# Performance work log

Measured on AMD Instinct MI355X. Metric: run time of the kernel, lower is better.

The kernel has to match this reference:

```python
import jax, jax.numpy as jnp
import numpy as np

D_MODEL, D_HEAD, N_HEAD = 1024, 64, 16
B, S = 8, 1024


def setup_inputs() -> dict:
    key = jax.random.key(0)
    ks = jax.random.split(key, 11)
    sc = 1.0 / np.sqrt(D_MODEL)
    inp = {
        "query": jax.random.normal(ks[0], (B, S, D_MODEL), jnp.float32),
        "key": jax.random.normal(ks[1], (B, S, D_MODEL), jnp.float32),
        "value": jax.random.normal(ks[2], (B, S, D_MODEL), jnp.float32),
        # stacked per-head Q/K projections: [H, d_model, d_head]
        "Wq": jax.random.normal(ks[3], (N_HEAD, D_MODEL, D_HEAD), jnp.float32) * sc,
        "bq": jax.random.normal(ks[4], (N_HEAD, D_HEAD), jnp.float32) * 0.01,
        "Wk": jax.random.normal(ks[5], (N_HEAD, D_MODEL, D_HEAD), jnp.float32) * sc,
        "bk": jax.random.normal(ks[6], (N_HEAD, D_HEAD), jnp.float32) * 0.01,
        # shared V projection
        "Wv": jax.random.normal(ks[7], (D_MODEL, D_HEAD), jnp.float32) * sc,
        "bv": jax.random.normal(ks[8], (D_HEAD,), jnp.float32) * 0.01,
        # output projection d_head -> d_model
        "Wo": jax.random.normal(ks[9], (D_HEAD, D_MODEL), jnp.float32) * (1.0 / np.sqrt(D_HEAD)),
        "bo": jax.random.normal(ks[10], (D_MODEL,), jnp.float32) * 0.01,
    }
    return inp


def reference(query, key, value, Wq, bq, Wk, bk, Wv, bv, Wo, bo):
    scale = D_HEAD ** -0.5
    # per-head projections, batched over heads: [B, H, S, d_head]
    Q = jnp.einsum("bsd,hdk->bhsk", query, Wq) + bq[None, :, None, :]
    K = jnp.einsum("bsd,hdk->bhsk", key, Wk) + bk[None, :, None, :]
    # shared V: [B, S, d_head]
    V = value @ Wv + bv
    # attention weights per head: [B, H, S, S]
    wei = jax.nn.softmax(jnp.einsum("bhsk,bhtk->bhst", Q, K) * scale, axis=-1)
    # head outputs averaged (shared V): [B, S, d_head]
    out = jnp.mean(jnp.einsum("bhst,btk->bhsk", wei, V), axis=1)
    return out @ Wo + bo
```

## Files before the change

kernel.cpp:

```cpp
#include <hip/hip_runtime.h>
#include <hip/hip_bf16.h>
#include <math.h>

typedef __attribute__((ext_vector_type(4))) float  f32x4;
typedef __attribute__((ext_vector_type(8))) __bf16 bf16x8;
typedef __attribute__((ext_vector_type(4))) __bf16 bf16x4;
typedef __attribute__((ext_vector_type(4))) short  s16x4;

#define SCL 0.18033688011111543f
#define MFMA16(a, b, c)   __builtin_amdgcn_mfma_f32_16x16x32_bf16((a), (b), (c), 0, 0, 0)
#define MFMA16K16(a, b, c) __builtin_amdgcn_mfma_f32_16x16x16bf16_1k((a), (b), (c), 0, 0, 0)

union B4 { bf16x4 b; s16x4 s; };

__device__ __forceinline__ float exp2_fast(float x) {
    float r;
    asm("v_exp_f32 %0, %1" : "=v"(r) : "v"(x));
    return r;
}

__device__ __forceinline__ void gload16(const __bf16* g, __bf16* l) {
    __builtin_amdgcn_global_load_lds(
        (const __attribute__((address_space(1))) void*)g,
        (__attribute__((address_space(3))) void*)l, 16, 0, 0);
}

__global__ __launch_bounds__(256) void pack_all(
    const float* __restrict__ Wq, const float* __restrict__ Wk,
    const float* __restrict__ Wv, const float* __restrict__ bv,
    const float* __restrict__ Wo,
    __bf16* __restrict__ WqT, __bf16* __restrict__ WkT,
    __bf16* __restrict__ WvT, float* __restrict__ bvP, __bf16* __restrict__ WoT)
{
    const int tid = threadIdx.x;
    if (blockIdx.x >= 256) {
        int idx = (blockIdx.x - 256) * 256 + tid;
        if (idx < 131072) {
            int n = idx >> 10, k = idx & 1023;
            WvT[idx] = (n < 64) ? (__bf16)Wv[k * 64 + n] : (__bf16)0.0f;
        }
        if (idx < 65536) {
            int n = idx >> 6, d = idx & 63;
            WoT[idx] = (__bf16)Wo[d * 1024 + n];
        }
        if (idx < 128) bvP[idx] = (idx < 64) ? bv[idx] : 0.0f;
        return;
    }
    __shared__ __bf16 T0[64][68];
    __shared__ __bf16 T1[64][68];
    const int h = blockIdx.x & 15, kt = blockIdx.x >> 4;
    const int kk = tid >> 2, cf = (tid & 3) * 16;
    const size_t base = (size_t)h * 65536 + (size_t)(kt * 64 + kk) * 64 + cf;
    #pragma unroll
    for (int j = 0; j < 4; ++j) {
        f32x4 v = *(const f32x4*)&Wq[base + 4 * j];
        f32x4 u = *(const f32x4*)&Wk[base + 4 * j];
        bf16x4 vb, ub;
        #pragma unroll
        for (int e = 0; e < 4; ++e) { vb[e] = (__bf16)v[e]; ub[e] = (__bf16)u[e]; }
        *(bf16x4*)&T0[kk][cf + 4 * j] = vb;
        *(bf16x4*)&T1[kk][cf + 4 * j] = ub;
    }
    __syncthreads();
    const int c = tid >> 2, k8 = (tid & 3) * 16;
    bf16x8 q0, q1, k0v, k1v;
    #pragma unroll
    for (int j = 0; j < 8; ++j) {
        q0[j] = T0[k8 + j][c];     q1[j] = T0[k8 + 8 + j][c];
        k0v[j] = T1[k8 + j][c];    k1v[j] = T1[k8 + 8 + j][c];
    }
    size_t dst = (size_t)(h * 64 + c) * 1024 + kt * 64 + k8;
    *(bf16x8*)&WqT[dst] = q0;  *(bf16x8*)&WqT[dst + 8] = q1;
    *(bf16x8*)&WkT[dst] = k0v; *(bf16x8*)&WkT[dst + 8] = k1v;
}

__global__ __launch_bounds__(256) void cvt2(
    const float* __restrict__ q, const float* __restrict__ k,
    __bf16* __restrict__ qb, __bf16* __restrict__ kb)
{
    size_t base = ((size_t)blockIdx.x * 256 + threadIdx.x) * 8;
    f32x4 a0 = *(const f32x4*)&q[base];
    f32x4 a1 = *(const f32x4*)&q[base + 4];
    f32x4 b0 = *(const f32x4*)&k[base];
    f32x4 b1 = *(const f32x4*)&k[base + 4];
    bf16x8 oq, ok;
    #pragma unroll
    for (int j = 0; j < 4; ++j) {
        oq[j] = (__bf16)a0[j]; oq[4 + j] = (__bf16)a1[j];
        ok[j] = (__bf16)b0[j]; ok[4 + j] = (__bf16)b1[j];
    }
    *(bf16x8*)&qb[base] = oq;
    *(bf16x8*)&kb[base] = ok;
}

__global__ __launch_bounds__(256, 4) void proj_qk(
    const __bf16* __restrict__ Aq, const __bf16* __restrict__ Ak,
    const __bf16* __restrict__ WqT, const __bf16* __restrict__ WkT,
    const float* __restrict__ bq, const float* __restrict__ bk,
    __bf16* __restrict__ Cq, __bf16* __restrict__ Ck)
{
    const int z = blockIdx.z;
    const __bf16* A  = z ? Ak : Aq;
    const __bf16* Bt = z ? WkT : WqT;
    const float* bias = z ? bk : bq;
    __bf16* C = z ? Ck : Cq;
    const float oscale = z ? 1.0f : SCL;

    __shared__ __bf16 As[128][64];
    __shared__ __bf16 Bs[128][64];

    const int tid = threadIdx.x;
    const int lane = tid & 63, w = tid >> 6;
    const int wr = w >> 1, wc = w & 1;
    const int l15 = lane & 15, g = lane >> 4;
    const int m0 = blockIdx.x * 128, n0 = blockIdx.y * 128;

    const int lrow8 = lane >> 3;
    const int slot  = (lane & 7) ^ lrow8;
    const int scol  = slot * 8;

    f32x4 acc[4][4] = {};

    for (int k0 = 0; k0 < 1024; k0 += 64) {
        #pragma unroll
        for (int c = 0; c < 4; ++c) {
            int row = w * 32 + c * 8 + lrow8;
            gload16(&A [(size_t)(m0 + row) * 1024 + k0 + scol], &As[0][0] + (w * 4 + c) * 512);
            gload16(&Bt[(size_t)(n0 + row) * 1024 + k0 + scol], &Bs[0][0] + (w * 4 + c) * 512);
        }
        __syncthreads();

        __builtin_amdgcn_s_setprio(1);
        #pragma unroll
        for (int ks = 0; ks < 2; ++ks) {
            bf16x8 af[4], bfv[4];
            #pragma unroll
            for (int mi = 0; mi < 4; ++mi) {
                int row = 64 * wr + 16 * mi + l15;
                af[mi] = *(const bf16x8*)((const char*)&As[0][0]
                            + row * 128 + (((4 * ks + g) ^ (row & 7)) << 4));
            }
            #pragma unroll
            for (int ni = 0; ni < 4; ++ni) {
                int row = 64 * wc + 16 * ni + l15;
                bfv[ni] = *(const bf16x8*)((const char*)&Bs[0][0]
                            + row * 128 + (((4 * ks + g) ^ (row & 7)) << 4));
            }
            #pragma unroll
            for (int mi = 0; mi < 4; ++mi)
                #pragma unroll
                for (int ni = 0; ni < 4; ++ni)
                    acc[mi][ni] = MFMA16(af[mi], bfv[ni], acc[mi][ni]);
        }
        __builtin_amdgcn_s_setprio(0);
        __syncthreads();
    }

    #pragma unroll
    for (int mi = 0; mi < 4; ++mi)
        #pragma unroll
        for (int ni = 0; ni < 4; ++ni) {
            int n = n0 + 64 * wc + 16 * ni + l15;
            float bn = bias[n];
            #pragma unroll
            for (int r = 0; r < 4; ++r) {
                int m = m0 + 64 * wr + 16 * mi + 4 * g + r;
                C[(size_t)m * 1024 + n] = (__bf16)((acc[mi][ni][r] + bn) * oscale);
            }
        }
}

__global__ __launch_bounds__(256, 2) void proj_v(
    const float* __restrict__ A, const __bf16* __restrict__ Bt,
    const float* __restrict__ bias, __bf16* __restrict__ C)
{
    __shared__ __bf16 As[2][64][72];
    __shared__ __bf16 Bs[2][64][72];

    const int tid = threadIdx.x;
    const int lane = tid & 63, w = tid >> 6;
    const int wr = w >> 1, wc = w & 1;
    const int l15 = lane & 15, g = lane >> 4;
    const int m0 = blockIdx.x * 64;
    const int arow = tid >> 2, acf = (tid & 3) * 16;
    const int bcf = (tid & 3) * 16;

    f32x4 areg[4];
    bf16x8 breg[2];
    #pragma unroll
    for (int j = 0; j < 4; ++j)
        areg[j] = *(const f32x4*)&A[(size_t)(m0 + arow) * 1024 + acf + 4 * j];
    #pragma unroll
    for (int j = 0; j < 2; ++j)
        breg[j] = *(const bf16x8*)&Bt[(size_t)arow * 1024 + bcf + 8 * j];

    f32x4 acc[2][2] = {};
    int cur = 0;
    for (int k0 = 0; k0 < 1024; k0 += 64) {
        #pragma unroll
        for (int j = 0; j < 4; ++j) {
            bf16x4 c4;
            #pragma unroll
            for (int e = 0; e < 4; ++e) c4[e] = (__bf16)areg[j][e];
            *(bf16x4*)&As[cur][arow][acf + 4 * j] = c4;
        }
        #pragma unroll
        for (int j = 0; j < 2; ++j)
            *(bf16x8*)&Bs[cur][arow][bcf + 8 * j] = breg[j];
        if (k0 < 960) {
            #pragma unroll
            for (int j = 0; j < 4; ++j)
                areg[j] = *(const f32x4*)&A[(size_t)(m0 + arow) * 1024 + k0 + 64 + acf + 4 * j];
            #pragma unroll
            for (int j = 0; j < 2; ++j)
                breg[j] = *(const bf16x8*)&Bt[(size_t)arow * 1024 + k0 + 64 + bcf + 8 * j];
        }
        __syncthreads();
        #pragma unroll
        for (int ks = 0; ks < 2; ++ks) {
            bf16x8 af[2], bfv[2];
            #pragma unroll
            for (int mi = 0; mi < 2; ++mi)
                af[mi] = *(const bf16x8*)&As[cur][32 * wr + 16 * mi + l15][32 * ks + 8 * g];
            #pragma unroll
            for (int ni = 0; ni < 2; ++ni)
                bfv[ni] = *(const bf16x8*)&Bs[cur][32 * wc + 16 * ni + l15][32 * ks + 8 * g];
            #pragma unroll
            for (int mi = 0; mi < 2; ++mi)
                #pragma unroll
                for (int ni = 0; ni < 2; ++ni)
                    acc[mi][ni] = MFMA16(af[mi], bfv[ni], acc[mi][ni]);
        }
        __syncthreads();
        cur ^= 1;
    }

    #pragma unroll
    for (int mi = 0; mi < 2; ++mi)
        #pragma unroll
        for (int ni = 0; ni < 2; ++ni) {
            int n = 32 * wc + 16 * ni + l15;
            float bn = bias[n];
            #pragma unroll
            for (int r = 0; r < 4; ++r) {
                int m = m0 + 32 * wr + 16 * mi + 4 * g + r;
                C[(size_t)n * 8192 + m] = (__bf16)(acc[mi][ni][r] + bn);
            }
        }
}

__global__ __launch_bounds__(128, 4) void attn_kernel(
    const __bf16* __restrict__ Qb, const __bf16* __restrict__ Kb,
    const __bf16* __restrict__ Vt, __bf16* __restrict__ Oh)
{
    __shared__ __bf16 Ks[2][32][68];
    __shared__ __bf16 Vs[2][64][44];

    const int qt = blockIdx.x, bh = blockIdx.y;
    const int b = bh >> 4, h = bh & 15;
    const int tid = threadIdx.x;
    const int lane = tid & 63, w = tid >> 6;
    const int l15 = lane & 15, g = lane >> 4;
    const int s0 = b * 1024 + qt * 64;

    const int krow = tid >> 2, kc = (tid & 3) * 16;
    const int vrow = tid >> 1, vc = (tid & 1) * 16;

    bf16x8 qf[2][2];
    #pragma unroll
    for (int mi = 0; mi < 2; ++mi)
        #pragma unroll
        for (int ks = 0; ks < 2; ++ks)
            qf[mi][ks] = *(const bf16x8*)
                &Qb[(size_t)(s0 + 32 * w + 16 * mi + l15) * 1024 + h * 64 + 32 * ks + 8 * g];

    const __bf16* Kbase = Kb + (size_t)(b * 1024) * 1024 + h * 64;
    const __bf16* Vbase = Vt + (size_t)b * 1024;

    bf16x8 kreg[2], vreg[2];
    #pragma unroll
    for (int j = 0; j < 2; ++j) {
        kreg[j] = *(const bf16x8*)&Kbase[(size_t)krow * 1024 + kc + 8 * j];
        vreg[j] = *(const bf16x8*)&Vbase[(size_t)vrow * 8192 + vc + 8 * j];
    }

    f32x4 acc_o[2][4] = {};
    float l_par[2] = {0.0f, 0.0f};

    int cur = 0;
    for (int it = 0; it < 32; ++it) {
        *(bf16x8*)&Ks[cur][krow][kc]     = kreg[0];
        *(bf16x8*)&Ks[cur][krow][kc + 8] = kreg[1];
        *(bf16x8*)&Vs[cur][vrow][vc]     = vreg[0];
        *(bf16x8*)&Vs[cur][vrow][vc + 8] = vreg[1];
        if (it < 31) {
            int t1 = (it + 1) * 32;
            #pragma unroll
            for (int j = 0; j < 2; ++j) {
                kreg[j] = *(const bf16x8*)&Kbase[(size_t)(t1 + krow) * 1024 + kc + 8 * j];
                vreg[j] = *(const bf16x8*)&Vbase[(size_t)vrow * 8192 + t1 + vc + 8 * j];
            }
        }
        __syncthreads();

        f32x4 pacc[2][2] = {};
        __builtin_amdgcn_s_setprio(1);
        #pragma unroll
        for (int ks = 0; ks < 2; ++ks) {
            bf16x8 kf[2];
            #pragma unroll
            for (int ni = 0; ni < 2; ++ni)
                kf[ni] = *(const bf16x8*)&Ks[cur][16 * ni + l15][32 * ks + 8 * g];
            #pragma unroll
            for (int mi = 0; mi < 2; ++mi)
                #pragma unroll
                for (int ni = 0; ni < 2; ++ni)
                    pacc[mi][ni] = MFMA16(kf[ni], qf[mi][ks], pacc[mi][ni]);
        }
        __builtin_amdgcn_s_setprio(0);

        s16x4 pb[2][2];
        #pragma unroll
        for (int mi = 0; mi < 2; ++mi) {
            float rs = 0.0f;
            #pragma unroll
            for (int ni = 0; ni < 2; ++ni) {
                B4 pk;
                #pragma unroll
                for (int r = 0; r < 4; ++r) {
                    float pv = exp2_fast(pacc[mi][ni][r]);
                    rs += pv;
                    pk.b[r] = (__bf16)pv;
                }
                pb[mi][ni] = pk.s;
            }
            l_par[mi] += rs;
        }

        __builtin_amdgcn_s_setprio(1);
        #pragma unroll
        for (int c = 0; c < 2; ++c) {
            s16x4 vf[4];
            #pragma unroll
            for (int nd = 0; nd < 4; ++nd) {
                B4 vv;
                vv.b = *(const bf16x4*)&Vs[cur][16 * nd + l15][16 * c + 4 * g];
                vf[nd] = vv.s;
            }
            #pragma unroll
            for (int mi = 0; mi < 2; ++mi)
                #pragma unroll
                for (int nd = 0; nd < 4; ++nd)
                    acc_o[mi][nd] = MFMA16K16(vf[nd], pb[mi][c], acc_o[mi][nd]);
        }
        __builtin_amdgcn_s_setprio(0);
        cur ^= 1;
    }

    #pragma unroll
    for (int mi = 0; mi < 2; ++mi) {
        float l = l_par[mi];
        l += __shfl_xor(l, 16);
        l += __shfl_xor(l, 32);
        float rl = 1.0f / l;
        int q = qt * 64 + 32 * w + 16 * mi + l15;
        #pragma unroll
        for (int nd = 0; nd < 4; ++nd) {
            bf16x4 ov;
            #pragma unroll
            for (int r = 0; r < 4; ++r) ov[r] = (__bf16)(acc_o[mi][nd][r] * rl);
            *(bf16x4*)&Oh[(size_t)(bh * 1024 + q) * 64 + 16 * nd + 4 * g] = ov;
        }
    }
}

__global__ __launch_bounds__(256) void mean_kernel(
    const __bf16* __restrict__ Oh, __bf16* __restrict__ Om)
{
    int idx = blockIdx.x * 256 + threadIdx.x;
    int m = idx >> 3, d8 = (idx & 7) * 8;
    int b = m >> 10, q = m & 1023;
    const __bf16* src = Oh + (size_t)(b * 16) * 65536 + (size_t)q * 64 + d8;
    float s[8] = {};
    #pragma unroll
    for (int h = 0; h < 16; ++h) {
        bf16x8 v = *(const bf16x8*)&src[(size_t)h * 65536];
        #pragma unroll
        for (int j = 0; j < 8; ++j) s[j] += (float)v[j];
    }
    bf16x8 o;
    #pragma unroll
    for (int j = 0; j < 8; ++j) o[j] = (__bf16)(s[j] * 0.0625f);
    *(bf16x8*)&Om[(size_t)m * 64 + d8] = o;
}

__global__ __launch_bounds__(256, 4) void out_gemm(
    const __bf16* __restrict__ Om, const __bf16* __restrict__ WoT,
    const float* __restrict__ bo, float* __restrict__ out)
{
    const int tid = threadIdx.x;
    const int lane = tid & 63, w = tid >> 6;
    const int wr = w >> 1, wc = w & 1;
    const int l15 = lane & 15, g = lane >> 4;
    const int m0 = blockIdx.x * 128, n0 = blockIdx.y * 128;

    f32x4 acc[4][4] = {};
    #pragma unroll
    for (int ks = 0; ks < 2; ++ks) {
        bf16x8 af[4], bfv[4];
        #pragma unroll
        for (int mi = 0; mi < 4; ++mi)
            af[mi] = *(const bf16x8*)&Om[(size_t)(m0 + 64 * wr + 16 * mi + l15) * 64 + 32 * ks + 8 * g];
        #pragma unroll
        for (int ni = 0; ni < 4; ++ni)
            bfv[ni] = *(const bf16x8*)&WoT[(size_t)(n0 + 64 * wc + 16 * ni + l15) * 64 + 32 * ks + 8 * g];
        #pragma unroll
        for (int mi = 0; mi < 4; ++mi)
            #pragma unroll
            for (int ni = 0; ni < 4; ++ni)
                acc[mi][ni] = MFMA16(af[mi], bfv[ni], acc[mi][ni]);
    }
    #pragma unroll
    for (int mi = 0; mi < 4; ++mi)
        #pragma unroll
        for (int ni = 0; ni < 4; ++ni) {
            int n = n0 + 64 * wc + 16 * ni + l15;
            float bn = bo[n];
            #pragma unroll
            for (int r = 0; r < 4; ++r) {
                int m = m0 + 64 * wr + 16 * mi + 4 * g + r;
                out[(size_t)m * 1024 + n] = acc[mi][ni][r] + bn;
            }
        }
}

extern "C" void kernel_launch(void* const* d_in, const int* in_sizes, int n_in,
                              void* d_out, int out_size, void* d_ws, size_t ws_size,
                              hipStream_t stream)
{
    const float* query = (const float*)d_in[0];
    const float* key_  = (const float*)d_in[1];
    const float* value = (const float*)d_in[2];
    const float* Wq = (const float*)d_in[3];
    const float* bq = (const float*)d_in[4];
    const float* Wk = (const float*)d_in[5];
    const float* bk = (const float*)d_in[6];
    const float* Wv = (const float*)d_in[7];
    const float* bv = (const float*)d_in[8];
    const float* Wo = (const float*)d_in[9];
    const float* bo = (const float*)d_in[10];
    float* out = (float*)d_out;

    char* p = (char*)d_ws;
    __bf16* Qbuf = (__bf16*)p; p += 8192ull * 1024 * 2;
    __bf16* Kbuf = (__bf16*)p; p += 8192ull * 1024 * 2;
    __bf16* VtB  = (__bf16*)p; p += 64ull * 8192 * 2;
    __bf16* WqT  = (__bf16*)p; p += 1024ull * 1024 * 2;
    __bf16* WkT  = (__bf16*)p; p += 1024ull * 1024 * 2;
    __bf16* WvT  = (__bf16*)p; p += 128ull * 1024 * 2;
    __bf16* WoT  = (__bf16*)p; p += 1024ull * 64 * 2;
    float*  bvP  = (float*)p;  p += 128 * 4;
    __bf16* Oh   = (__bf16*)p; p += 8ull * 16 * 1024 * 64 * 2;
    __bf16* Om   = (__bf16*)p; p += 8192ull * 64 * 2;
    __bf16* Qa   = (__bf16*)p; p += 8192ull * 1024 * 2;
    __bf16* Ka   = (__bf16*)p; p += 8192ull * 1024 * 2;

    pack_all<<<768, 256, 0, stream>>>(Wq, Wk, Wv, bv, Wo, WqT, WkT, WvT, bvP, WoT);
    cvt2<<<4096, 256, 0, stream>>>(query, key_, Qa, Ka);
    proj_qk<<<dim3(64, 8, 2), 256, 0, stream>>>(Qa, Ka, WqT, WkT, bq, bk, Qbuf, Kbuf);
    proj_v<<<128, 256, 0, stream>>>(value, WvT, bvP, VtB);
    attn_kernel<<<dim3(16, 128), 128, 0, stream>>>(Qbuf, Kbuf, VtB, Oh);
    mean_kernel<<<256, 256, 0, stream>>>(Oh, Om);
    out_gemm<<<dim3(64, 8), 256, 0, stream>>>(Om, WoT, bo, out);
}
```

Baseline: 143.8 us.

## Fuse fp32-to-bf16 input conversion into Q/K projection GEMM with register prefetch

Drops the separate cvt2 kernel and its bf16 staging buffers. proj_qk now reads fp32 query/key directly, converts them to bf16 in registers, and stores them into a padded LDS tile. The next k-tile of A is prefetched into registers while the current one computes. This removes a full read-write round trip of the converted inputs and one launch. In exchange, every projection block re-reads the fp32 inputs (eight column blocks per row tile), so it moves more global bytes per tile and uses more registers.

```diff
diff --git a/kernel.cpp b/kernel.cpp
--- a/kernel.cpp
+++ b/kernel.cpp
@@ -74,39 +74,20 @@
     *(bf16x8*)&WkT[dst] = k0v; *(bf16x8*)&WkT[dst + 8] = k1v;
 }
 
-__global__ __launch_bounds__(256) void cvt2(
-    const float* __restrict__ q, const float* __restrict__ k,
-    __bf16* __restrict__ qb, __bf16* __restrict__ kb)
-{
-    size_t base = ((size_t)blockIdx.x * 256 + threadIdx.x) * 8;
-    f32x4 a0 = *(const f32x4*)&q[base];
-    f32x4 a1 = *(const f32x4*)&q[base + 4];
-    f32x4 b0 = *(const f32x4*)&k[base];
-    f32x4 b1 = *(const f32x4*)&k[base + 4];
-    bf16x8 oq, ok;
-    #pragma unroll
-    for (int j = 0; j < 4; ++j) {
-        oq[j] = (__bf16)a0[j]; oq[4 + j] = (__bf16)a1[j];
-        ok[j] = (__bf16)b0[j]; ok[4 + j] = (__bf16)b1[j];
-    }
-    *(bf16x8*)&qb[base] = oq;
-    *(bf16x8*)&kb[base] = ok;
-}
-
 __global__ __launch_bounds__(256, 4) void proj_qk(
-    const __bf16* __restrict__ Aq, const __bf16* __restrict__ Ak,
+    const float* __restrict__ Aq, const float* __restrict__ Ak,
     const __bf16* __restrict__ WqT, const __bf16* __restrict__ WkT,
     const float* __restrict__ bq, const float* __restrict__ bk,
     __bf16* __restrict__ Cq, __bf16* __restrict__ Ck)
 {
     const int z = blockIdx.z;
-    const __bf16* A  = z ? Ak : Aq;
+    const float* A   = z ? Ak : Aq;
     const __bf16* Bt = z ? WkT : WqT;
     const float* bias = z ? bk : bq;
     __bf16* C = z ? Ck : Cq;
     const float oscale = z ? 1.0f : SCL;
 
-    __shared__ __bf16 As[128][64];
+    __shared__ __bf16 As[128][72];
     __shared__ __bf16 Bs[128][64];
 
     const int tid = threadIdx.x;
@@ -115,19 +96,42 @@
     const int l15 = lane & 15, g = lane >> 4;
     const int m0 = blockIdx.x * 128, n0 = blockIdx.y * 128;
 
+    const int arow = tid >> 2, acf = (tid & 3) * 16;
     const int lrow8 = lane >> 3;
     const int slot  = (lane & 7) ^ lrow8;
     const int scol  = slot * 8;
 
+    bf16x8 abf[4];
+    auto loadA = [&](int k0) {
+        #pragma unroll
+        for (int half = 0; half < 2; ++half)
+            #pragma unroll
+            for (int j2 = 0; j2 < 2; ++j2) {
+                const float* src = &A[(size_t)(m0 + arow + 64 * half) * 1024 + k0 + acf + 8 * j2];
+                f32x4 v0 = *(const f32x4*)src;
+                f32x4 v1 = *(const f32x4*)(src + 4);
+                bf16x8 o;
+                #pragma unroll
+                for (int e = 0; e < 4; ++e) { o[e] = (__bf16)v0[e]; o[4 + e] = (__bf16)v1[e]; }
+                abf[half * 2 + j2] = o;
+            }
+    };
+    loadA(0);
+
     f32x4 acc[4][4] = {};
 
     for (int k0 = 0; k0 < 1024; k0 += 64) {
+        #pragma unroll
+        for (int half = 0; half < 2; ++half)
+            #pragma unroll
+            for (int j2 = 0; j2 < 2; ++j2)
+                *(bf16x8*)&As[arow + 64 * half][acf + 8 * j2] = abf[half * 2 + j2];
         #pragma unroll
         for (int c = 0; c < 4; ++c) {
             int row = w * 32 + c * 8 + lrow8;
-            gload16(&A [(size_t)(m0 + row) * 1024 + k0 + scol], &As[0][0] + (w * 4 + c) * 512);
             gload16(&Bt[(size_t)(n0 + row) * 1024 + k0 + scol], &Bs[0][0] + (w * 4 + c) * 512);
         }
+        if (k0 < 960) loadA(k0 + 64);
         __syncthreads();
 
         __builtin_amdgcn_s_setprio(1);
@@ -135,11 +139,8 @@
         for (int ks = 0; ks < 2; ++ks) {
             bf16x8 af[4], bfv[4];
             #pragma unroll
-            for (int mi = 0; mi < 4; ++mi) {
-                int row = 64 * wr + 16 * mi + l15;
-                af[mi] = *(const bf16x8*)((const char*)&As[0][0]
-                            + row * 128 + (((4 * ks + g) ^ (row & 7)) << 4));
-            }
+            for (int mi = 0; mi < 4; ++mi)
+                af[mi] = *(const bf16x8*)&As[64 * wr + 16 * mi + l15][32 * ks + 8 * g];
             #pragma unroll
             for (int ni = 0; ni < 4; ++ni) {
                 int row = 64 * wc + 16 * ni + l15;
@@ -462,12 +463,9 @@
     float*  bvP  = (float*)p;  p += 128 * 4;
     __bf16* Oh   = (__bf16*)p; p += 8ull * 16 * 1024 * 64 * 2;
     __bf16* Om   = (__bf16*)p; p += 8192ull * 64 * 2;
-    __bf16* Qa   = (__bf16*)p; p += 8192ull * 1024 * 2;
-    __bf16* Ka   = (__bf16*)p; p += 8192ull * 1024 * 2;
 
     pack_all<<<768, 256, 0, stream>>>(Wq, Wk, Wv, bv, Wo, WqT, WkT, WvT, bvP, WoT);
-    cvt2<<<4096, 256, 0, stream>>>(query, key_, Qa, Ka);
-    proj_qk<<<dim3(64, 8, 2), 256, 0, stream>>>(Qa, Ka, WqT, WkT, bq, bk, Qbuf, Kbuf);
+    proj_qk<<<dim3(64, 8, 2), 256, 0, stream>>>(query, key_, WqT, WkT, bq, bk, Qbuf, Kbuf);
     proj_v<<<128, 256, 0, stream>>>(value, WvT, bvP, VtB);
     attn_kernel<<<dim3(16, 128), 128, 0, stream>>>(Qbuf, Kbuf, VtB, Oh);
     mean_kernel<<<256, 256, 0, stream>>>(Oh, Om);
```

New measurement: 147.0 us. 1.02x slower.

## Fuse input conversion into pack kernel and remap workgroups for XCD L2 locality

Applied to the files above, without the earlier changes.

Merges the cvt2 float-to-bf16 conversion of query/key into the pack_all weight-packing launch as extra blocks, removing one kernel launch. It also remaps workgroup IDs in proj_qk and attn_kernel so that consecutive logical tiles land on the same XCD (round-robin by 8), letting blocks that share K/V or weight tiles reuse the same L2. The remap is a bijection only when the grid sizes are multiples of 8, which holds for the current launch shapes.

```diff
diff --git a/kernel.cpp b/kernel.cpp
--- a/kernel.cpp
+++ b/kernel.cpp
@@ -29,10 +29,28 @@
     const float* __restrict__ Wq, const float* __restrict__ Wk,
     const float* __restrict__ Wv, const float* __restrict__ bv,
     const float* __restrict__ Wo,
+    const float* __restrict__ query, const float* __restrict__ key_,
     __bf16* __restrict__ WqT, __bf16* __restrict__ WkT,
-    __bf16* __restrict__ WvT, float* __restrict__ bvP, __bf16* __restrict__ WoT)
+    __bf16* __restrict__ WvT, float* __restrict__ bvP, __bf16* __restrict__ WoT,
+    __bf16* __restrict__ Qa, __bf16* __restrict__ Ka)
 {
     const int tid = threadIdx.x;
+    if (blockIdx.x >= 768) {
+        size_t base = ((size_t)(blockIdx.x - 768) * 256 + tid) * 8;
+        f32x4 a0 = *(const f32x4*)&query[base];
+        f32x4 a1 = *(const f32x4*)&query[base + 4];
+        f32x4 b0 = *(const f32x4*)&key_[base];
+        f32x4 b1 = *(const f32x4*)&key_[base + 4];
+        bf16x8 oq, ok;
+        #pragma unroll
+        for (int j = 0; j < 4; ++j) {
+            oq[j] = (__bf16)a0[j]; oq[4 + j] = (__bf16)a1[j];
+            ok[j] = (__bf16)b0[j]; ok[4 + j] = (__bf16)b1[j];
+        }
+        *(bf16x8*)&Qa[base] = oq;
+        *(bf16x8*)&Ka[base] = ok;
+        return;
+    }
     if (blockIdx.x >= 256) {
         int idx = (blockIdx.x - 256) * 256 + tid;
         if (idx < 131072) {
@@ -72,25 +90,6 @@
     size_t dst = (size_t)(h * 64 + c) * 1024 + kt * 64 + k8;
     *(bf16x8*)&WqT[dst] = q0;  *(bf16x8*)&WqT[dst + 8] = q1;
     *(bf16x8*)&WkT[dst] = k0v; *(bf16x8*)&WkT[dst + 8] = k1v;
-}
-
-__global__ __launch_bounds__(256) void cvt2(
-    const float* __restrict__ q, const float* __restrict__ k,
-    __bf16* __restrict__ qb, __bf16* __restrict__ kb)
-{
-    size_t base = ((size_t)blockIdx.x * 256 + threadIdx.x) * 8;
-    f32x4 a0 = *(const f32x4*)&q[base];
-    f32x4 a1 = *(const f32x4*)&q[base + 4];
-    f32x4 b0 = *(const f32x4*)&k[base];
-    f32x4 b1 = *(const f32x4*)&k[base + 4];
-    bf16x8 oq, ok;
-    #pragma unroll
-    for (int j = 0; j < 4; ++j) {
-        oq[j] = (__bf16)a0[j]; oq[4 + j] = (__bf16)a1[j];
-        ok[j] = (__bf16)b0[j]; ok[4 + j] = (__bf16)b1[j];
-    }
-    *(bf16x8*)&qb[base] = oq;
-    *(bf16x8*)&kb[base] = ok;
 }
 
 __global__ __launch_bounds__(256, 4) void proj_qk(
@@ -113,7 +112,10 @@
     const int lane = tid & 63, w = tid >> 6;
     const int wr = w >> 1, wc = w & 1;
     const int l15 = lane & 15, g = lane >> 4;
-    const int m0 = blockIdx.x * 128, n0 = blockIdx.y * 128;
+
+    const int wg  = blockIdx.x + 64 * blockIdx.y;
+    const int nid = (wg & 7) * 64 + (wg >> 3);
+    const int m0 = (nid & 63) * 128, n0 = (nid >> 6) * 128;
 
     const int lrow8 = lane >> 3;
     const int slot  = (lane & 7) ^ lrow8;
@@ -256,7 +258,9 @@
     __shared__ __bf16 Ks[2][32][68];
     __shared__ __bf16 Vs[2][64][44];
 
-    const int qt = blockIdx.x, bh = blockIdx.y;
+    const int wg  = blockIdx.x + 16 * blockIdx.y;
+    const int nid = (wg & 7) * 256 + (wg >> 3);
+    const int qt = nid & 15, bh = nid >> 4;
     const int b = bh >> 4, h = bh & 15;
     const int tid = threadIdx.x;
     const int lane = tid & 63, w = tid >> 6;
@@ -465,8 +469,8 @@
     __bf16* Qa   = (__bf16*)p; p += 8192ull * 1024 * 2;
     __bf16* Ka   = (__bf16*)p; p += 8192ull * 1024 * 2;
 
-    pack_all<<<768, 256, 0, stream>>>(Wq, Wk, Wv, bv, Wo, WqT, WkT, WvT, bvP, WoT);
-    cvt2<<<4096, 256, 0, stream>>>(query, key_, Qa, Ka);
+    pack_all<<<4864, 256, 0, stream>>>(Wq, Wk, Wv, bv, Wo, query, key_,
+                                       WqT, WkT, WvT, bvP, WoT, Qa, Ka);
     proj_qk<<<dim3(64, 8, 2), 256, 0, stream>>>(Qa, Ka, WqT, WkT, bq, bk, Qbuf, Kbuf);
     proj_v<<<128, 256, 0, stream>>>(value, WvT, bvP, VtB);
     attn_kernel<<<dim3(16, 128), 128, 0, stream>>>(Qbuf, Kbuf, VtB, Oh);
```

Measured after the change: 149.8 us. 4.2% more time.
